# Optimization experiments

Hardware: AMD Instinct MI355X
Metric: run time of the kernel (lower is better)

Reference implementation:

```python
import jax, jax.numpy as jnp
import numpy as np
import math

B, T, D = 2, 2048, 2048
H, HKV = 32, 8
DH = D // H          # 64
G = H // HKV         # 4 query heads per kv head
ROPE_BASE = 10000.0


def _rope_cos_sin(t, dh):
    inv_freq = 1.0 / (ROPE_BASE ** (jnp.arange(0, dh, 2, dtype=jnp.float32) / dh))
    pos = jnp.arange(t, dtype=jnp.float32)
    freqs = pos[:, None] * inv_freq[None, :]          # [T, Dh/2]
    emb = jnp.concatenate([freqs, freqs], axis=-1)    # [T, Dh]
    return jnp.cos(emb), jnp.sin(emb)


def _rotate_half(y):
    y1, y2 = jnp.split(y, 2, axis=-1)
    return jnp.concatenate([-y2, y1], axis=-1)


def _apply_rope(x, cos, sin):  # x: [..., T, Dh]; cos/sin: [T, Dh]
    return x * cos + _rotate_half(x) * sin


def setup_inputs() -> dict:
    key = jax.random.key(0)
    k = jax.random.split(key, 5)
    x = jax.random.normal(k[0], (B, T, D), dtype=jnp.float32)
    Wq = jax.random.normal(k[1], (D, D), dtype=jnp.float32) * 0.02
    Wk = jax.random.normal(k[2], (D, HKV * DH), dtype=jnp.float32) * 0.02
    Wv = jax.random.normal(k[3], (D, HKV * DH), dtype=jnp.float32) * 0.02
    Wo = jax.random.normal(k[4], (D, D), dtype=jnp.float32) * 0.02
    causal = jnp.tril(jnp.ones((T, T), dtype=bool))
    attn_mask = jnp.where(causal, 0.0, -1e9).astype(jnp.float32)[None, None]  # [1,1,T,T]
    return {"x": x, "Wq": Wq, "Wk": Wk, "Wv": Wv, "Wo": Wo, "attn_mask": attn_mask}


def reference(x, Wq, Wk, Wv, Wo, attn_mask):
    Bx, Tx, Dx = x.shape
    # projections (Linear, no bias)
    q = (x @ Wq).reshape(Bx, Tx, H, DH).transpose(0, 2, 1, 3)      # [B,H,T,Dh]
    kk = (x @ Wk).reshape(Bx, Tx, HKV, DH).transpose(0, 2, 1, 3)   # [B,Hkv,T,Dh]
    vv = (x @ Wv).reshape(Bx, Tx, HKV, DH).transpose(0, 2, 1, 3)   # [B,Hkv,T,Dh]
    # RoPE on q and k (offset=0, no kv cache)
    cos, sin = _rope_cos_sin(Tx, DH)
    q = _apply_rope(q, cos, sin)
    kk = _apply_rope(kk, cos, sin)
    # GQA: group query heads so head h uses kv head h // G (matches repeat_interleave)
    qg = q.reshape(Bx, HKV, G, Tx, DH)
    att = jnp.einsum('bkgtd,bksd->bkgts', qg, kk) / math.sqrt(DH)
    att = att + attn_mask[:, :, None]                              # broadcast over groups
    p = jax.nn.softmax(att, axis=-1)
    ctx = jnp.einsum('bkgts,bksd->bkgtd', p, vv)                   # [B,Hkv,G,T,Dh]
    ctx = ctx.reshape(Bx, H, Tx, DH).transpose(0, 2, 1, 3).reshape(Bx, Tx, Dx)
    return ctx @ Wo
```

## Files before the change

### kernel.cpp

```cpp
#include <hip/hip_runtime.h>
#include <hip/hip_bf16.h>


typedef __bf16 bf16_t;
typedef __bf16 bf16x4 __attribute__((ext_vector_type(4)));
typedef __bf16 bf16x8 __attribute__((ext_vector_type(8)));
typedef float f32x4 __attribute__((ext_vector_type(4)));

#define B_ 2
#define T_ 2048
#define D_ 2048
#define H_ 32
#define HKV_ 8
#define DH_ 64

__device__ __forceinline__ float fast_exp2(float x) { return __builtin_amdgcn_exp2f(x); }

__device__ __forceinline__ void gld_lds16(const bf16_t* g, bf16_t* l) {
  __builtin_amdgcn_global_load_lds((const __attribute__((address_space(1))) unsigned int*)g,
                                   (__attribute__((address_space(3))) unsigned int*)l, 16, 0, 0);
}

__global__ __launch_bounds__(256) void cast_f32_bf16(const float* __restrict__ in,
                                                     bf16_t* __restrict__ out, int n) {
  int i = (blockIdx.x * 256 + threadIdx.x) * 8;
  if (i < n) {
    f32x4 a = *(const f32x4*)&in[i];
    f32x4 b = *(const f32x4*)&in[i + 4];
    bf16x8 o;
    o[0] = (bf16_t)a[0]; o[1] = (bf16_t)a[1]; o[2] = (bf16_t)a[2]; o[3] = (bf16_t)a[3];
    o[4] = (bf16_t)b[0]; o[5] = (bf16_t)b[1]; o[6] = (bf16_t)b[2]; o[7] = (bf16_t)b[3];
    *(bf16x8*)&out[i] = o;
  }
}

__global__ __launch_bounds__(256) void transpose_w(const float* __restrict__ W,
                                                   bf16_t* __restrict__ Wt, int K, int N) {
  __shared__ float tile[64][65];
  int n0 = blockIdx.x * 64, k0 = blockIdx.y * 64;
  int tid = threadIdx.x;
  for (int i = tid; i < 4096; i += 256) {
    int r = i >> 6, c = i & 63;
    tile[r][c] = W[(size_t)(k0 + r) * N + n0 + c];
  }
  __syncthreads();
  for (int i = tid; i < 4096; i += 256) {
    int r = i >> 6, c = i & 63;
    Wt[(size_t)(n0 + r) * K + k0 + c] = (bf16_t)tile[c][r];
  }
}

__global__ __launch_bounds__(256) void transpose_wqkv(const float* __restrict__ Wq,
                                                      const float* __restrict__ Wk,
                                                      const float* __restrict__ Wv,
                                                      bf16_t* __restrict__ Wt) {
  __shared__ float tile[64][65];
  int n0 = blockIdx.x * 64, k0 = blockIdx.y * 64;
  const float* W;
  int srcN, col;
  if (n0 < 2048) { W = Wq; srcN = 2048; col = n0; }
  else if (n0 < 2560) { W = Wk; srcN = 512; col = n0 - 2048; }
  else { W = Wv; srcN = 512; col = n0 - 2560; }
  int tid = threadIdx.x;
  for (int i = tid; i < 4096; i += 256) {
    int r = i >> 6, c = i & 63;
    tile[r][c] = W[(size_t)(k0 + r) * srcN + col + c];
  }
  __syncthreads();
  for (int i = tid; i < 4096; i += 256) {
    int r = i >> 6, c = i & 63;
    Wt[(size_t)(n0 + r) * 2048 + k0 + c] = (bf16_t)tile[c][r];
  }
}

template <typename OutT>
__global__ __launch_bounds__(256) void gemm_bt(const bf16_t* __restrict__ A,
                                               const bf16_t* __restrict__ Bt,
                                               OutT* __restrict__ C, int M, int N, int K) {
  __shared__ __align__(16) bf16_t As[2 * 128 * 32];
  __shared__ __align__(16) bf16_t Bs[2 * 128 * 32];
  int tid = threadIdx.x;
  int lane = tid & 63;
  int wave = tid >> 6;
  int l15 = lane & 15;
  int quad = lane >> 4;
  int m0 = blockIdx.y * 128;
  int n0 = blockIdx.x * 128;
  int wrow = (wave >> 1) * 64;
  int wcol = (wave & 1) * 64;

  f32x4 acc[4][4] = {};

  for (int kc = 0; kc < K; kc += 64) {
#pragma unroll
    for (int kk = 0; kk < 2; ++kk) {
#pragma unroll
      for (int c = 0; c < 2; ++c) {
        int linear = c * 256 + tid;
        int r = linear >> 2, seg = linear & 3;
        gld_lds16(&A[(size_t)(m0 + r) * K + kc + kk * 32 + seg * 8],
                  &As[kk * 4096 + (size_t)(c * 256 + wave * 64) * 8]);
        gld_lds16(&Bt[(size_t)(n0 + r) * K + kc + kk * 32 + seg * 8],
                  &Bs[kk * 4096 + (size_t)(c * 256 + wave * 64) * 8]);
      }
    }
    __syncthreads();
#pragma unroll
    for (int kk = 0; kk < 2; ++kk) {
      bf16x8 af[4], bfr[4];
#pragma unroll
      for (int mi = 0; mi < 4; ++mi)
        af[mi] = *(const bf16x8*)&As[kk * 4096 + (wrow + mi * 16 + l15) * 32 + quad * 8];
#pragma unroll
      for (int ni = 0; ni < 4; ++ni)
        bfr[ni] = *(const bf16x8*)&Bs[kk * 4096 + (wcol + ni * 16 + l15) * 32 + quad * 8];
#pragma unroll
      for (int mi = 0; mi < 4; ++mi)
#pragma unroll
        for (int ni = 0; ni < 4; ++ni)
          acc[mi][ni] = __builtin_amdgcn_mfma_f32_16x16x32_bf16(af[mi], bfr[ni], acc[mi][ni], 0, 0, 0);
    }
    __syncthreads();
  }
#pragma unroll
  for (int mi = 0; mi < 4; ++mi) {
#pragma unroll
    for (int ni = 0; ni < 4; ++ni) {
#pragma unroll
      for (int r = 0; r < 4; ++r) {
        int m = m0 + wrow + mi * 16 + quad * 4 + r;
        int n = n0 + wcol + ni * 16 + l15;
        C[(size_t)m * N + n] = (OutT)acc[mi][ni][r];
      }
    }
  }
}

__global__ __launch_bounds__(256) void rope_qk(const bf16_t* __restrict__ qkv,
                                               bf16_t* __restrict__ qr,
                                               bf16_t* __restrict__ kr) {
  int t = blockIdx.x, b = blockIdx.y;
  int tid = threadIdx.x;
  const bf16_t* row = qkv + (size_t)(b * T_ + t) * 3072;
  const float LN1E4_over32 = 9.210340371976184f / 32.0f;
  const float QSC = 1.44269504088896f * 0.125f;
  for (int i = tid; i < 1024 + 256; i += 256) {
    bool isq = i < 1024;
    int ii = isq ? i : i - 1024;
    int hh = ii >> 5, j = ii & 31;
    int base = isq ? 0 : 2048;
    float inv = __expf(-(float)j * LN1E4_over32);
    float fr = (float)t * inv;
    float sn, cs;
    sincosf(fr, &sn, &cs);
    float x1 = (float)row[base + hh * 64 + j];
    float x2 = (float)row[base + hh * 64 + j + 32];
    float o1 = x1 * cs - x2 * sn;
    float o2 = x2 * cs + x1 * sn;
    if (isq) {
      size_t o = ((size_t)(b * H_ + hh) * T_ + t) * DH_;
      qr[o + j] = (bf16_t)(o1 * QSC);
      qr[o + j + 32] = (bf16_t)(o2 * QSC);
    } else {
      size_t o = ((size_t)(b * HKV_ + hh) * T_ + t) * DH_;
      kr[o + j] = (bf16_t)o1;
      kr[o + j + 32] = (bf16_t)o2;
    }
  }
}

__global__ __launch_bounds__(256) void transpose_v(const bf16_t* __restrict__ qkv,
                                                   bf16_t* __restrict__ vtr) {
  __shared__ __align__(16) bf16_t tile[64][72];
  int t0 = blockIdx.x * 64;
  int hk = blockIdx.y;
  int b = blockIdx.z;
  int tid = threadIdx.x;
  for (int i = tid; i < 512; i += 256) {
    int r = i >> 3, s = i & 7;
    *(bf16x8*)&tile[r][s * 8] =
        *(const bf16x8*)&qkv[(size_t)(b * T_ + t0 + r) * 3072 + 2560 + hk * 64 + s * 8];
  }
  __syncthreads();
  for (int i = tid; i < 4096; i += 256) {
    int dd = i >> 6, tt = i & 63;
    int src = (tt & 32) | ((tt & 4) << 2) | ((tt & 24) >> 1) | (tt & 3);
    vtr[((size_t)(b * HKV_ + hk) * DH_ + dd) * T_ + t0 + tt] = tile[src][dd];
  }
}

#define DO_HALF(QF, O, LACC, DOMASK, KS, VT)                                           \
  {                                                                                    \
    f32x4 s_[4] = {};                                                                  \
    _Pragma("unroll") for (int mt = 0; mt < 4; ++mt) {                                 \
      bf16x8 ak0 = *(const bf16x8*)&KS[(mt * 16 + l15) * 72 + quad * 8];               \
      bf16x8 ak1 = *(const bf16x8*)&KS[(mt * 16 + l15) * 72 + 32 + quad * 8];          \
      s_[mt] = __builtin_amdgcn_mfma_f32_16x16x32_bf16(ak0, QF[0], s_[mt], 0, 0, 0);   \
      s_[mt] = __builtin_amdgcn_mfma_f32_16x16x32_bf16(ak1, QF[1], s_[mt], 0, 0, 0);   \
    }                                                                                  \
    if (DOMASK) {                                                                      \
      _Pragma("unroll") for (int mt = 0; mt < 4; ++mt)                                 \
          _Pragma("unroll") for (int r = 0; r < 4; ++r) if (mt * 16 + quad * 4 + r >   \
                                                            wave * 16 + l15)           \
              s_[mt][r] = -1e30f;                                                      \
    }                                                                                  \
    _Pragma("unroll") for (int k0 = 0; k0 < 2; ++k0) {                                 \
      bf16x8 pa;                                                                       \
      _Pragma("unroll") for (int hh = 0; hh < 2; ++hh)                                 \
          _Pragma("unroll") for (int r = 0; r < 4; ++r) {                              \
        float p = fast_exp2(s_[2 * k0 + hh][r]);                                       \
        LACC += p;                                                                     \
        pa[hh * 4 + r] = (bf16_t)p;                                                    \
      }                                                                                \
      _Pragma("unroll") for (int dn = 0; dn < 4; ++dn) {                               \
        bf16x8 bv = *(const bf16x8*)&VT[(dn * 16 + l15) * 72 + k0 * 32 + quad * 8];    \
        O[dn] = __builtin_amdgcn_mfma_f32_16x16x32_bf16(pa, bv, O[dn], 0, 0, 0);       \
      }                                                                                \
    }                                                                                  \
  }

__global__ __launch_bounds__(256) void flash_attn(const bf16_t* __restrict__ qr,
                                                  const bf16_t* __restrict__ kr,
                                                  const bf16_t* __restrict__ vtr,
                                                  bf16_t* __restrict__ ctxb) {
  __shared__ __align__(16) bf16_t Ks[2][64 * 72];
  __shared__ __align__(16) bf16_t Vt[2][64 * 72];
  int tid = threadIdx.x;
  int lane = tid & 63;
  int wave = tid >> 6;
  int l15 = lane & 15, quad = lane >> 4;
  int pair = blockIdx.x, h = blockIdx.y, b = blockIdx.z;
  int qtA = pair, qtB = 31 - pair;
  int nkvA = qtA + 1, nkvB = qtB + 1;
  int kvh = h >> 2;

  const bf16_t* qbA = qr + ((size_t)(b * H_ + h) * T_ + qtA * 64 + wave * 16) * DH_;
  const bf16_t* qbB = qr + ((size_t)(b * H_ + h) * T_ + qtB * 64 + wave * 16) * DH_;
  const bf16_t* kbase = kr + (size_t)(b * HKV_ + kvh) * T_ * DH_;
  const bf16_t* vbase = vtr + (size_t)(b * HKV_ + kvh) * DH_ * T_;

  bf16x8 qA[2], qB[2];
#pragma unroll
  for (int k0 = 0; k0 < 2; ++k0) {
    qA[k0] = *(const bf16x8*)&qbA[l15 * 64 + k0 * 32 + quad * 8];
    qB[k0] = *(const bf16x8*)&qbB[l15 * 64 + k0 * 32 + quad * 8];
  }

  f32x4 oA[4] = {}, oB[4] = {};
  float lA = 0.f, lB = 0.f;

  bf16x8 kreg[2], vreg[2];
  auto load_kv = [&](int kv) {
#pragma unroll
    for (int c = 0; c < 2; ++c) {
      int idx = c * 256 + tid;
      int r = idx >> 3, sg = idx & 7;
      kreg[c] = *(const bf16x8*)&kbase[(size_t)kv * 4096 + r * 64 + sg * 8];
      vreg[c] = *(const bf16x8*)&vbase[(size_t)r * T_ + kv * 64 + sg * 8];
    }
  };
  load_kv(0);

  for (int kv = 0; kv < nkvB; ++kv) {
    bf16_t* ks = Ks[kv & 1];
    bf16_t* vt = Vt[kv & 1];
#pragma unroll
    for (int c = 0; c < 2; ++c) {
      int idx = c * 256 + tid;
      int r = idx >> 3, sg = idx & 7;
      *(bf16x8*)&ks[r * 72 + sg * 8] = kreg[c];
      *(bf16x8*)&vt[r * 72 + sg * 8] = vreg[c];
    }
    __syncthreads();
    if (kv + 1 < nkvB) load_kv(kv + 1);

    DO_HALF(qB, oB, lB, kv == qtB, ks, vt);
    if (kv < nkvA) DO_HALF(qA, oA, lA, kv == qtA, ks, vt);
  }

  lA += __shfl_xor(lA, 16, 64);
  lA += __shfl_xor(lA, 32, 64);
  lB += __shfl_xor(lB, 16, 64);
  lB += __shfl_xor(lB, 32, 64);
  float invA = 1.0f / lA, invB = 1.0f / lB;
#pragma unroll
  for (int r = 0; r < 4; ++r) {
    float iAr = __shfl(invA, quad * 4 + r, 64);
    float iBr = __shfl(invB, quad * 4 + r, 64);
    int tA = qtA * 64 + wave * 16 + quad * 4 + r;
    int tB = qtB * 64 + wave * 16 + quad * 4 + r;
#pragma unroll
    for (int dn = 0; dn < 4; ++dn) {
      ctxb[(size_t)(b * T_ + tA) * D_ + h * 64 + dn * 16 + l15] = (bf16_t)(oA[dn][r] * iAr);
      ctxb[(size_t)(b * T_ + tB) * D_ + h * 64 + dn * 16 + l15] = (bf16_t)(oB[dn][r] * iBr);
    }
  }
}

extern "C" void kernel_launch(void* const* d_in, const int* in_sizes, int n_in,
                              void* d_out, int out_size, void* d_ws, size_t ws_size,
                              hipStream_t stream) {
  const float* x = (const float*)d_in[0];
  const float* Wq = (const float*)d_in[1];
  const float* Wk = (const float*)d_in[2];
  const float* Wv = (const float*)d_in[3];
  const float* Wo = (const float*)d_in[4];
  float* out = (float*)d_out;

  char* ws = (char*)d_ws;
  size_t off = 0;
  bf16_t* xb = (bf16_t*)(ws + off); off += (size_t)B_ * T_ * D_ * 2;
  bf16_t* wqkvb = (bf16_t*)(ws + off); off += (size_t)3072 * 2048 * 2;
  bf16_t* wob = (bf16_t*)(ws + off); off += (size_t)2048 * 2048 * 2;
  bf16_t* qkv = (bf16_t*)(ws + off); off += (size_t)4096 * 3072 * 2;
  bf16_t* qr = (bf16_t*)(ws + off); off += (size_t)B_ * H_ * T_ * DH_ * 2;
  bf16_t* kr = (bf16_t*)(ws + off); off += (size_t)B_ * HKV_ * T_ * DH_ * 2;
  bf16_t* vtr = (bf16_t*)(ws + off); off += (size_t)B_ * HKV_ * T_ * DH_ * 2;
  bf16_t* ctxb = (bf16_t*)(ws + off); off += (size_t)B_ * T_ * D_ * 2;

  int nx = B_ * T_ * D_;
  cast_f32_bf16<<<nx / 8 / 256, 256, 0, stream>>>(x, xb, nx);
  transpose_wqkv<<<dim3(3072 / 64, 2048 / 64), 256, 0, stream>>>(Wq, Wk, Wv, wqkvb);
  transpose_w<<<dim3(2048 / 64, 2048 / 64), 256, 0, stream>>>(Wo, wob, 2048, 2048);

  gemm_bt<bf16_t><<<dim3(3072 / 128, 4096 / 128), 256, 0, stream>>>(xb, wqkvb, qkv, 4096, 3072, 2048);

  rope_qk<<<dim3(T_, B_), 256, 0, stream>>>(qkv, qr, kr);
  transpose_v<<<dim3(T_ / 64, HKV_, B_), 256, 0, stream>>>(qkv, vtr);

  flash_attn<<<dim3(16, H_, B_), 256, 0, stream>>>(qr, kr, vtr, ctxb);

  gemm_bt<float><<<dim3(2048 / 128, 4096 / 128), 256, 0, stream>>>(ctxb, wob, out, 4096, 2048, 2048);
}
```

Measured before the change: 317.3 us.

## Enlarge flash-attention query tile to 128 rows per tile, two row groups per wave

Each wave now handles 32 query rows (two 16-row groups) instead of 16, so each block covers a pair of 128-row query tiles and the grid shrinks from 16 to 8 blocks along the pair axis. Every K/V tile staged in LDS and every K/V fragment read from LDS now feeds twice as many MFMAs, which cuts global and LDS traffic per unit of compute. The cost is more registers for accumulators and Q fragments, and half as many blocks in the grid. The causal mask is now applied to the last two KV tiles of each query tile using absolute positions.

```diff
diff --git a/kernel.cpp b/kernel.cpp
--- a/kernel.cpp
+++ b/kernel.cpp
@@ -189,36 +189,6 @@
   }
 }
 
-#define DO_HALF(QF, O, LACC, DOMASK, KS, VT)                                           \
-  {                                                                                    \
-    f32x4 s_[4] = {};                                                                  \
-    _Pragma("unroll") for (int mt = 0; mt < 4; ++mt) {                                 \
-      bf16x8 ak0 = *(const bf16x8*)&KS[(mt * 16 + l15) * 72 + quad * 8];               \
-      bf16x8 ak1 = *(const bf16x8*)&KS[(mt * 16 + l15) * 72 + 32 + quad * 8];          \
-      s_[mt] = __builtin_amdgcn_mfma_f32_16x16x32_bf16(ak0, QF[0], s_[mt], 0, 0, 0);   \
-      s_[mt] = __builtin_amdgcn_mfma_f32_16x16x32_bf16(ak1, QF[1], s_[mt], 0, 0, 0);   \
-    }                                                                                  \
-    if (DOMASK) {                                                                      \
-      _Pragma("unroll") for (int mt = 0; mt < 4; ++mt)                                 \
-          _Pragma("unroll") for (int r = 0; r < 4; ++r) if (mt * 16 + quad * 4 + r >   \
-                                                            wave * 16 + l15)           \
-              s_[mt][r] = -1e30f;                                                      \
-    }                                                                                  \
-    _Pragma("unroll") for (int k0 = 0; k0 < 2; ++k0) {                                 \
-      bf16x8 pa;                                                                       \
-      _Pragma("unroll") for (int hh = 0; hh < 2; ++hh)                                 \
-          _Pragma("unroll") for (int r = 0; r < 4; ++r) {                              \
-        float p = fast_exp2(s_[2 * k0 + hh][r]);                                       \
-        LACC += p;                                                                     \
-        pa[hh * 4 + r] = (bf16_t)p;                                                    \
-      }                                                                                \
-      _Pragma("unroll") for (int dn = 0; dn < 4; ++dn) {                               \
-        bf16x8 bv = *(const bf16x8*)&VT[(dn * 16 + l15) * 72 + k0 * 32 + quad * 8];    \
-        O[dn] = __builtin_amdgcn_mfma_f32_16x16x32_bf16(pa, bv, O[dn], 0, 0, 0);       \
-      }                                                                                \
-    }                                                                                  \
-  }
-
 __global__ __launch_bounds__(256) void flash_attn(const bf16_t* __restrict__ qr,
                                                   const bf16_t* __restrict__ kr,
                                                   const bf16_t* __restrict__ vtr,
@@ -230,24 +200,28 @@
   int wave = tid >> 6;
   int l15 = lane & 15, quad = lane >> 4;
   int pair = blockIdx.x, h = blockIdx.y, b = blockIdx.z;
-  int qtA = pair, qtB = 31 - pair;
-  int nkvA = qtA + 1, nkvB = qtB + 1;
+  int qtA = pair, qtB = 15 - pair;
+  int nkvA = 2 * qtA + 2, nkvB = 2 * qtB + 2;
   int kvh = h >> 2;
 
-  const bf16_t* qbA = qr + ((size_t)(b * H_ + h) * T_ + qtA * 64 + wave * 16) * DH_;
-  const bf16_t* qbB = qr + ((size_t)(b * H_ + h) * T_ + qtB * 64 + wave * 16) * DH_;
+  const bf16_t* qbase = qr + (size_t)(b * H_ + h) * T_ * DH_;
   const bf16_t* kbase = kr + (size_t)(b * HKV_ + kvh) * T_ * DH_;
   const bf16_t* vbase = vtr + (size_t)(b * HKV_ + kvh) * DH_ * T_;
 
-  bf16x8 qA[2], qB[2];
-#pragma unroll
-  for (int k0 = 0; k0 < 2; ++k0) {
-    qA[k0] = *(const bf16x8*)&qbA[l15 * 64 + k0 * 32 + quad * 8];
-    qB[k0] = *(const bf16x8*)&qbB[l15 * 64 + k0 * 32 + quad * 8];
-  }
-
-  f32x4 oA[4] = {}, oB[4] = {};
-  float lA = 0.f, lB = 0.f;
+  int rowA = qtA * 128 + wave * 32;
+  int rowB = qtB * 128 + wave * 32;
+
+  bf16x8 qA[2][2], qB[2][2];
+#pragma unroll
+  for (int rg = 0; rg < 2; ++rg)
+#pragma unroll
+    for (int k0 = 0; k0 < 2; ++k0) {
+      qA[rg][k0] = *(const bf16x8*)&qbase[(size_t)(rowA + rg * 16 + l15) * 64 + k0 * 32 + quad * 8];
+      qB[rg][k0] = *(const bf16x8*)&qbase[(size_t)(rowB + rg * 16 + l15) * 64 + k0 * 32 + quad * 8];
+    }
+
+  f32x4 oA[2][4] = {}, oB[2][4] = {};
+  float lA0 = 0.f, lA1 = 0.f, lB0 = 0.f, lB1 = 0.f;
 
   bf16x8 kreg[2], vreg[2];
   auto load_kv = [&](int kv) {
@@ -274,25 +248,113 @@
     __syncthreads();
     if (kv + 1 < nkvB) load_kv(kv + 1);
 
-    DO_HALF(qB, oB, lB, kv == qtB, ks, vt);
-    if (kv < nkvA) DO_HALF(qA, oA, lA, kv == qtA, ks, vt);
-  }
-
-  lA += __shfl_xor(lA, 16, 64);
-  lA += __shfl_xor(lA, 32, 64);
-  lB += __shfl_xor(lB, 16, 64);
-  lB += __shfl_xor(lB, 32, 64);
-  float invA = 1.0f / lA, invB = 1.0f / lB;
+    bool actA = kv < nkvA;
+
+    f32x4 sA[2][4] = {}, sB[2][4] = {};
+#pragma unroll
+    for (int mt = 0; mt < 4; ++mt) {
+      bf16x8 ak0 = *(const bf16x8*)&ks[(mt * 16 + l15) * 72 + quad * 8];
+      bf16x8 ak1 = *(const bf16x8*)&ks[(mt * 16 + l15) * 72 + 32 + quad * 8];
+#pragma unroll
+      for (int rg = 0; rg < 2; ++rg) {
+        sB[rg][mt] = __builtin_amdgcn_mfma_f32_16x16x32_bf16(ak0, qB[rg][0], sB[rg][mt], 0, 0, 0);
+        sB[rg][mt] = __builtin_amdgcn_mfma_f32_16x16x32_bf16(ak1, qB[rg][1], sB[rg][mt], 0, 0, 0);
+      }
+      if (actA) {
+#pragma unroll
+        for (int rg = 0; rg < 2; ++rg) {
+          sA[rg][mt] = __builtin_amdgcn_mfma_f32_16x16x32_bf16(ak0, qA[rg][0], sA[rg][mt], 0, 0, 0);
+          sA[rg][mt] = __builtin_amdgcn_mfma_f32_16x16x32_bf16(ak1, qA[rg][1], sA[rg][mt], 0, 0, 0);
+        }
+      }
+    }
+
+    int ct = kv * 64;
+    if (kv >= 2 * qtB) {
+#pragma unroll
+      for (int rg = 0; rg < 2; ++rg)
+#pragma unroll
+        for (int mt = 0; mt < 4; ++mt)
+#pragma unroll
+          for (int r = 0; r < 4; ++r)
+            if (ct + mt * 16 + quad * 4 + r > rowB + rg * 16 + l15) sB[rg][mt][r] = -1e30f;
+    }
+    if (actA && kv >= 2 * qtA) {
+#pragma unroll
+      for (int rg = 0; rg < 2; ++rg)
+#pragma unroll
+        for (int mt = 0; mt < 4; ++mt)
+#pragma unroll
+          for (int r = 0; r < 4; ++r)
+            if (ct + mt * 16 + quad * 4 + r > rowA + rg * 16 + l15) sA[rg][mt][r] = -1e30f;
+    }
+
+    bf16x8 paA[2][2], paB[2][2];
+#pragma unroll
+    for (int rg = 0; rg < 2; ++rg)
+#pragma unroll
+      for (int k0 = 0; k0 < 2; ++k0)
+#pragma unroll
+        for (int hh = 0; hh < 2; ++hh)
+#pragma unroll
+          for (int r = 0; r < 4; ++r) {
+            float p = fast_exp2(sB[rg][2 * k0 + hh][r]);
+            if (rg == 0) lB0 += p; else lB1 += p;
+            paB[rg][k0][hh * 4 + r] = (bf16_t)p;
+          }
+    if (actA) {
+#pragma unroll
+      for (int rg = 0; rg < 2; ++rg)
+#pragma unroll
+        for (int k0 = 0; k0 < 2; ++k0)
+#pragma unroll
+          for (int hh = 0; hh < 2; ++hh)
+#pragma unroll
+            for (int r = 0; r < 4; ++r) {
+              float p = fast_exp2(sA[rg][2 * k0 + hh][r]);
+              if (rg == 0) lA0 += p; else lA1 += p;
+              paA[rg][k0][hh * 4 + r] = (bf16_t)p;
+            }
+    }
+
+#pragma unroll
+    for (int k0 = 0; k0 < 2; ++k0) {
+#pragma unroll
+      for (int dn = 0; dn < 4; ++dn) {
+        bf16x8 bv = *(const bf16x8*)&vt[(dn * 16 + l15) * 72 + k0 * 32 + quad * 8];
+#pragma unroll
+        for (int rg = 0; rg < 2; ++rg)
+          oB[rg][dn] = __builtin_amdgcn_mfma_f32_16x16x32_bf16(paB[rg][k0], bv, oB[rg][dn], 0, 0, 0);
+        if (actA) {
+#pragma unroll
+          for (int rg = 0; rg < 2; ++rg)
+            oA[rg][dn] = __builtin_amdgcn_mfma_f32_16x16x32_bf16(paA[rg][k0], bv, oA[rg][dn], 0, 0, 0);
+        }
+      }
+    }
+  }
+
+  lA0 += __shfl_xor(lA0, 16, 64); lA0 += __shfl_xor(lA0, 32, 64);
+  lA1 += __shfl_xor(lA1, 16, 64); lA1 += __shfl_xor(lA1, 32, 64);
+  lB0 += __shfl_xor(lB0, 16, 64); lB0 += __shfl_xor(lB0, 32, 64);
+  lB1 += __shfl_xor(lB1, 16, 64); lB1 += __shfl_xor(lB1, 32, 64);
+  float iA0 = 1.0f / lA0, iA1 = 1.0f / lA1, iB0 = 1.0f / lB0, iB1 = 1.0f / lB1;
 #pragma unroll
   for (int r = 0; r < 4; ++r) {
-    float iAr = __shfl(invA, quad * 4 + r, 64);
-    float iBr = __shfl(invB, quad * 4 + r, 64);
-    int tA = qtA * 64 + wave * 16 + quad * 4 + r;
-    int tB = qtB * 64 + wave * 16 + quad * 4 + r;
+    float vA0 = __shfl(iA0, quad * 4 + r, 64);
+    float vA1 = __shfl(iA1, quad * 4 + r, 64);
+    float vB0 = __shfl(iB0, quad * 4 + r, 64);
+    float vB1 = __shfl(iB1, quad * 4 + r, 64);
+    int tA0 = rowA + quad * 4 + r;
+    int tA1 = rowA + 16 + quad * 4 + r;
+    int tB0 = rowB + quad * 4 + r;
+    int tB1 = rowB + 16 + quad * 4 + r;
 #pragma unroll
     for (int dn = 0; dn < 4; ++dn) {
-      ctxb[(size_t)(b * T_ + tA) * D_ + h * 64 + dn * 16 + l15] = (bf16_t)(oA[dn][r] * iAr);
-      ctxb[(size_t)(b * T_ + tB) * D_ + h * 64 + dn * 16 + l15] = (bf16_t)(oB[dn][r] * iBr);
+      ctxb[(size_t)(b * T_ + tA0) * D_ + h * 64 + dn * 16 + l15] = (bf16_t)(oA[0][dn][r] * vA0);
+      ctxb[(size_t)(b * T_ + tA1) * D_ + h * 64 + dn * 16 + l15] = (bf16_t)(oA[1][dn][r] * vA1);
+      ctxb[(size_t)(b * T_ + tB0) * D_ + h * 64 + dn * 16 + l15] = (bf16_t)(oB[0][dn][r] * vB0);
+      ctxb[(size_t)(b * T_ + tB1) * D_ + h * 64 + dn * 16 + l15] = (bf16_t)(oB[1][dn][r] * vB1);
     }
   }
 }
@@ -328,7 +390,7 @@
   rope_qk<<<dim3(T_, B_), 256, 0, stream>>>(qkv, qr, kr);
   transpose_v<<<dim3(T_ / 64, HKV_, B_), 256, 0, stream>>>(qkv, vtr);
 
-  flash_attn<<<dim3(16, H_, B_), 256, 0, stream>>>(qr, kr, vtr, ctxb);
+  flash_attn<<<dim3(8, H_, B_), 256, 0, stream>>>(qr, kr, vtr, ctxb);
 
   gemm_bt<float><<<dim3(2048 / 128, 4096 / 128), 256, 0, stream>>>(ctxb, wob, out, 4096, 2048, 2048);
 }
```

New measurement: 352.5 us. 1.11x slower.

## Stage K/V tiles via direct global-to-LDS loads with pre-swizzled layouts

Applied to the files above, without the earlier changes.

The flash attention kernel now loads K and transposed-V tiles straight from global memory into LDS with global_load_lds, instead of going through registers and then storing to LDS. The padded 72-wide LDS rows become unpadded 64-wide rows. To avoid bank conflicts without padding, the rope and V-transpose kernels write K and V to global memory with an XOR swizzle on the column index, and the attention reads undo it with a per-lane XOR. The goal is to cut register pressure and LDS store instructions in the main loop. It relies on the barrier waiting for the asynchronous LDS loads, and it makes the intermediate K/V layouts depend on this kernel.

```diff
diff --git a/kernel.cpp b/kernel.cpp
--- a/kernel.cpp
+++ b/kernel.cpp
@@ -144,6 +144,7 @@
   const bf16_t* row = qkv + (size_t)(b * T_ + t) * 3072;
   const float LN1E4_over32 = 9.210340371976184f / 32.0f;
   const float QSC = 1.44269504088896f * 0.125f;
+  int ksw = (t & 7) << 3;
   for (int i = tid; i < 1024 + 256; i += 256) {
     bool isq = i < 1024;
     int ii = isq ? i : i - 1024;
@@ -163,8 +164,8 @@
       qr[o + j + 32] = (bf16_t)(o2 * QSC);
     } else {
       size_t o = ((size_t)(b * HKV_ + hh) * T_ + t) * DH_;
-      kr[o + j] = (bf16_t)o1;
-      kr[o + j + 32] = (bf16_t)o2;
+      kr[o + (j ^ ksw)] = (bf16_t)o1;
+      kr[o + ((j + 32) ^ ksw)] = (bf16_t)o2;
     }
   }
 }
@@ -185,50 +186,53 @@
   for (int i = tid; i < 4096; i += 256) {
     int dd = i >> 6, tt = i & 63;
     int src = (tt & 32) | ((tt & 4) << 2) | ((tt & 24) >> 1) | (tt & 3);
-    vtr[((size_t)(b * HKV_ + hk) * DH_ + dd) * T_ + t0 + tt] = tile[src][dd];
-  }
-}
-
-#define DO_HALF(QF, O, LACC, DOMASK, KS, VT)                                           \
-  {                                                                                    \
-    f32x4 s_[4] = {};                                                                  \
-    _Pragma("unroll") for (int mt = 0; mt < 4; ++mt) {                                 \
-      bf16x8 ak0 = *(const bf16x8*)&KS[(mt * 16 + l15) * 72 + quad * 8];               \
-      bf16x8 ak1 = *(const bf16x8*)&KS[(mt * 16 + l15) * 72 + 32 + quad * 8];          \
-      s_[mt] = __builtin_amdgcn_mfma_f32_16x16x32_bf16(ak0, QF[0], s_[mt], 0, 0, 0);   \
-      s_[mt] = __builtin_amdgcn_mfma_f32_16x16x32_bf16(ak1, QF[1], s_[mt], 0, 0, 0);   \
-    }                                                                                  \
-    if (DOMASK) {                                                                      \
-      _Pragma("unroll") for (int mt = 0; mt < 4; ++mt)                                 \
-          _Pragma("unroll") for (int r = 0; r < 4; ++r) if (mt * 16 + quad * 4 + r >   \
-                                                            wave * 16 + l15)           \
-              s_[mt][r] = -1e30f;                                                      \
-    }                                                                                  \
-    _Pragma("unroll") for (int k0 = 0; k0 < 2; ++k0) {                                 \
-      bf16x8 pa;                                                                       \
-      _Pragma("unroll") for (int hh = 0; hh < 2; ++hh)                                 \
-          _Pragma("unroll") for (int r = 0; r < 4; ++r) {                              \
-        float p = fast_exp2(s_[2 * k0 + hh][r]);                                       \
-        LACC += p;                                                                     \
-        pa[hh * 4 + r] = (bf16_t)p;                                                    \
-      }                                                                                \
-      _Pragma("unroll") for (int dn = 0; dn < 4; ++dn) {                               \
-        bf16x8 bv = *(const bf16x8*)&VT[(dn * 16 + l15) * 72 + k0 * 32 + quad * 8];    \
-        O[dn] = __builtin_amdgcn_mfma_f32_16x16x32_bf16(pa, bv, O[dn], 0, 0, 0);       \
-      }                                                                                \
-    }                                                                                  \
+    int dst = tt ^ ((dd & 7) << 3);
+    vtr[((size_t)(b * HKV_ + hk) * DH_ + dd) * T_ + t0 + dst] = tile[src][dd];
+  }
+}
+
+#define DO_HALF(QF, O, LACC, DOMASK, KS, VT)                                              \
+  {                                                                                       \
+    f32x4 s_[4] = {};                                                                     \
+    _Pragma("unroll") for (int mt = 0; mt < 4; ++mt) {                                    \
+      bf16x8 ak0 = *(const bf16x8*)&KS[(mt * 16 + l15) * 64 + ((quad * 8) ^ swz)];        \
+      bf16x8 ak1 = *(const bf16x8*)&KS[(mt * 16 + l15) * 64 + ((32 + quad * 8) ^ swz)];   \
+      s_[mt] = __builtin_amdgcn_mfma_f32_16x16x32_bf16(ak0, QF[0], s_[mt], 0, 0, 0);      \
+      s_[mt] = __builtin_amdgcn_mfma_f32_16x16x32_bf16(ak1, QF[1], s_[mt], 0, 0, 0);      \
+    }                                                                                     \
+    if (DOMASK) {                                                                         \
+      _Pragma("unroll") for (int mt = 0; mt < 4; ++mt)                                    \
+          _Pragma("unroll") for (int r = 0; r < 4; ++r) if (mt * 16 + quad * 4 + r >      \
+                                                            wave * 16 + l15)              \
+              s_[mt][r] = -1e30f;                                                         \
+    }                                                                                     \
+    _Pragma("unroll") for (int k0 = 0; k0 < 2; ++k0) {                                    \
+      bf16x8 pa;                                                                          \
+      _Pragma("unroll") for (int hh = 0; hh < 2; ++hh)                                    \
+          _Pragma("unroll") for (int r = 0; r < 4; ++r) {                                 \
+        float p = fast_exp2(s_[2 * k0 + hh][r]);                                          \
+        LACC += p;                                                                        \
+        pa[hh * 4 + r] = (bf16_t)p;                                                       \
+      }                                                                                   \
+      _Pragma("unroll") for (int dn = 0; dn < 4; ++dn) {                                  \
+        bf16x8 bv =                                                                       \
+            *(const bf16x8*)&VT[(dn * 16 + l15) * 64 + ((k0 * 32 + quad * 8) ^ swz)];     \
+        O[dn] = __builtin_amdgcn_mfma_f32_16x16x32_bf16(pa, bv, O[dn], 0, 0, 0);          \
+      }                                                                                   \
+    }                                                                                     \
   }
 
 __global__ __launch_bounds__(256) void flash_attn(const bf16_t* __restrict__ qr,
                                                   const bf16_t* __restrict__ kr,
                                                   const bf16_t* __restrict__ vtr,
                                                   bf16_t* __restrict__ ctxb) {
-  __shared__ __align__(16) bf16_t Ks[2][64 * 72];
-  __shared__ __align__(16) bf16_t Vt[2][64 * 72];
+  __shared__ __align__(16) bf16_t Ks[2][64 * 64];
+  __shared__ __align__(16) bf16_t Vt[2][64 * 64];
   int tid = threadIdx.x;
   int lane = tid & 63;
   int wave = tid >> 6;
   int l15 = lane & 15, quad = lane >> 4;
+  int swz = (l15 & 7) * 8;
   int pair = blockIdx.x, h = blockIdx.y, b = blockIdx.z;
   int qtA = pair, qtB = 31 - pair;
   int nkvA = qtA + 1, nkvB = qtB + 1;
@@ -249,30 +253,23 @@
   f32x4 oA[4] = {}, oB[4] = {};
   float lA = 0.f, lB = 0.f;
 
-  bf16x8 kreg[2], vreg[2];
-  auto load_kv = [&](int kv) {
+  auto stage = [&](int kv, int bf) {
 #pragma unroll
     for (int c = 0; c < 2; ++c) {
       int idx = c * 256 + tid;
-      int r = idx >> 3, sg = idx & 7;
-      kreg[c] = *(const bf16x8*)&kbase[(size_t)kv * 4096 + r * 64 + sg * 8];
-      vreg[c] = *(const bf16x8*)&vbase[(size_t)r * T_ + kv * 64 + sg * 8];
+      bf16_t* dst = &Ks[bf][(c * 256 + wave * 64) * 8];
+      gld_lds16(&kbase[(size_t)kv * 4096 + idx * 8], dst);
+      bf16_t* dstv = &Vt[bf][(c * 256 + wave * 64) * 8];
+      gld_lds16(&vbase[(size_t)(idx >> 3) * T_ + kv * 64 + (idx & 7) * 8], dstv);
     }
   };
-  load_kv(0);
+  stage(0, 0);
 
   for (int kv = 0; kv < nkvB; ++kv) {
-    bf16_t* ks = Ks[kv & 1];
-    bf16_t* vt = Vt[kv & 1];
-#pragma unroll
-    for (int c = 0; c < 2; ++c) {
-      int idx = c * 256 + tid;
-      int r = idx >> 3, sg = idx & 7;
-      *(bf16x8*)&ks[r * 72 + sg * 8] = kreg[c];
-      *(bf16x8*)&vt[r * 72 + sg * 8] = vreg[c];
-    }
+    const bf16_t* ks = Ks[kv & 1];
+    const bf16_t* vt = Vt[kv & 1];
     __syncthreads();
-    if (kv + 1 < nkvB) load_kv(kv + 1);
+    if (kv + 1 < nkvB) stage(kv + 1, (kv + 1) & 1);
 
     DO_HALF(qB, oB, lB, kv == qtB, ks, vt);
     if (kv < nkvA) DO_HALF(qA, oA, lA, kv == qtA, ks, vt);
```

Measured after the change: 324.8 us. 1.02x slower.
